# Kernel optimization log

Measured on AMD Instinct MI355X. Metric: run time of the kernel, lower is better.

Reference implementation:

```python
import jax, jax.numpy as jnp
import numpy as np
from functools import partial

L, B, E, H, NL = 512, 16, 768, 12, 12
D = E // H  # head dim = 64
FF = 4 * E
LN_EPS = 1e-5


def gelu_new(x):
    # HF openai-gpt ACT_FNS['gelu'] (tanh approximation)
    c = np.sqrt(2.0 / np.pi).astype(np.float32)
    return 0.5 * x * (1.0 + jnp.tanh(c * (x + 0.044715 * x * x * x)))


def layer_norm(x, g, b):
    mu = jnp.mean(x, axis=-1, keepdims=True)
    var = jnp.mean(jnp.square(x - mu), axis=-1, keepdims=True)
    return (x - mu) * jax.lax.rsqrt(var + LN_EPS) * g + b


def setup_inputs() -> dict:
    key = jax.random.key(0)
    ks = jax.random.split(key, 8)
    s = 0.02
    x = jax.random.normal(ks[0], (L, B, E), dtype=jnp.float32)
    custom_mask = jnp.ones((B, L), dtype=jnp.float32)
    pos_emb = s * jax.random.normal(ks[1], (L, E), dtype=jnp.float32)
    # stacked per-layer params (leading axis = layer)
    params = {
        'c_attn_w': s * jax.random.normal(ks[2], (NL, E, 3 * E), dtype=jnp.float32),
        'c_attn_b': jnp.zeros((NL, 3 * E), dtype=jnp.float32),
        'attn_proj_w': s * jax.random.normal(ks[3], (NL, E, E), dtype=jnp.float32),
        'attn_proj_b': jnp.zeros((NL, E), dtype=jnp.float32),
        'ln1_g': jnp.ones((NL, E), dtype=jnp.float32),
        'ln1_b': jnp.zeros((NL, E), dtype=jnp.float32),
        'c_fc_w': s * jax.random.normal(ks[4], (NL, E, FF), dtype=jnp.float32),
        'c_fc_b': jnp.zeros((NL, FF), dtype=jnp.float32),
        'mlp_proj_w': s * jax.random.normal(ks[5], (NL, FF, E), dtype=jnp.float32),
        'mlp_proj_b': jnp.zeros((NL, E), dtype=jnp.float32),
        'ln2_g': jnp.ones((NL, E), dtype=jnp.float32),
        'ln2_b': jnp.zeros((NL, E), dtype=jnp.float32),
    }
    return {'x': x, 'custom_mask': custom_mask, 'pos_emb': pos_emb, **params}


def _gpt_forward(x, custom_mask, pos_emb, c_attn_w, c_attn_b, attn_proj_w,
                 attn_proj_b, ln1_g, ln1_b, c_fc_w, c_fc_b, mlp_proj_w,
                 mlp_proj_b, ln2_g, ln2_b):
    Lx, Bx, Ex = x.shape
    h = x.transpose(1, 0, 2) + pos_emb[None, :Lx]  # (B, L, E); dropout = eval identity
    # additive padding mask: (1 - m) * finfo.min, broadcast over heads/queries
    add_mask = (1.0 - custom_mask)[:, None, None, :] * jnp.finfo(jnp.float32).min
    causal = jnp.tril(jnp.ones((Lx, Lx), dtype=jnp.float32))  # bias buffer b

    def block(h, p):
        (caw, cab, apw, apb, g1, b1, fw, fb, pw, pb, g2, b2) = p
        qkv = h @ caw + cab                              # (B, L, 3E)
        q, k, v = jnp.split(qkv, 3, axis=-1)
        q = q.reshape(Bx, Lx, H, D).transpose(0, 2, 1, 3)  # (B, H, L, D)
        k = k.reshape(Bx, Lx, H, D).transpose(0, 2, 1, 3)
        v = v.reshape(Bx, Lx, H, D).transpose(0, 2, 1, 3)
        w = jnp.einsum('bhqd,bhkd->bhqk', q, k) / np.float32(np.sqrt(D))
        w = w * causal + (-10000.0) * (1.0 - causal)     # causal bias masking
        w = w + add_mask
        a = jax.nn.softmax(w, axis=-1)
        o = jnp.einsum('bhqk,bhkd->bhqd', a, v)          # (B, H, L, D)
        o = o.transpose(0, 2, 1, 3).reshape(Bx, Lx, Ex)
        a_out = o @ apw + apb
        n = layer_norm(h + a_out, g1, b1)
        m = gelu_new(n @ fw + fb) @ pw + pb
        h2 = layer_norm(n + m, g2, b2)
        return h2, None

    params = (c_attn_w, c_attn_b, attn_proj_w, attn_proj_b, ln1_g, ln1_b,
              c_fc_w, c_fc_b, mlp_proj_w, mlp_proj_b, ln2_g, ln2_b)
    h, _ = jax.lax.scan(block, h, params)
    return h.transpose(1, 0, 2)  # back to (L, B, E)


def reference(x, custom_mask, pos_emb, c_attn_w, c_attn_b, attn_proj_w,
              attn_proj_b, ln1_g, ln1_b, c_fc_w, c_fc_b, mlp_proj_w,
              mlp_proj_b, ln2_g, ln2_b):
    return _gpt_forward(x, custom_mask, pos_emb, c_attn_w, c_attn_b,
                        attn_proj_w, attn_proj_b, ln1_g, ln1_b, c_fc_w,
                        c_fc_b, mlp_proj_w, mlp_proj_b, ln2_g, ln2_b)
```

## Files before the change

### kernel.cpp

```cpp
#include <hip/hip_runtime.h>
#include <cstdint>
#include <cstddef>


#define LSEQ 512
#define NBATCH 16
#define EDIM 768
#define NHEAD 12
#define NLAYER 12

typedef __attribute__((ext_vector_type(8))) short short8;
typedef __attribute__((ext_vector_type(4))) float f32x4;

__device__ __forceinline__ short f2bf(float f) {
  union { float f; unsigned u; } x; x.f = f;
  return (short)((x.u + 0x7FFFu + ((x.u >> 16) & 1u)) >> 16);
}

__device__ __forceinline__ void gload_lds16(const void* g, void* l) {
  __builtin_amdgcn_global_load_lds(
      (__attribute__((address_space(1))) void*)(void*)g,
      (__attribute__((address_space(3))) void*)l, 16, 0, 0);
}

__global__ __launch_bounds__(256) void wt_transpose(const float* __restrict__ W,
                                                    short* __restrict__ Wt,
                                                    int K, int N) {
  __shared__ float tile[32][33];
  const int n0 = blockIdx.x * 32, k0 = blockIdx.y * 32;
  const size_t lo = (size_t)blockIdx.z * K * N;
  const float* Ws = W + lo;
  short* Wd = Wt + lo;
  const int tx = threadIdx.x & 31, ty = threadIdx.x >> 5;
#pragma unroll
  for (int i = 0; i < 4; ++i)
    tile[ty + i * 8][tx] = Ws[(size_t)(k0 + ty + i * 8) * N + n0 + tx];
  __syncthreads();
#pragma unroll
  for (int i = 0; i < 4; ++i)
    Wd[(size_t)(n0 + ty + i * 8) * K + k0 + tx] = f2bf(tile[tx][ty + i * 8]);
}

__global__ __launch_bounds__(256) void embed_k(const float* __restrict__ x,
                                               const float* __restrict__ pos,
                                               float* __restrict__ h,
                                               short* __restrict__ hbf) {
  const int row = blockIdx.x;
  const int b = row >> 9, lp = row & 511;
  const int t = threadIdx.x;
#pragma unroll
  for (int i = 0; i < 3; ++i) {
    const int e = t + i * 256;
    float v = x[(size_t)(lp * 16 + b) * 768 + e] + pos[(size_t)lp * 768 + e];
    h[(size_t)row * 768 + e] = v;
    hbf[(size_t)row * 768 + e] = f2bf(v);
  }
}

__global__ __launch_bounds__(256) void final_k(const float* __restrict__ h,
                                               float* __restrict__ out) {
  const int row = blockIdx.x;
  const int lp = row >> 4, b = row & 15;
  const int t = threadIdx.x;
#pragma unroll
  for (int i = 0; i < 3; ++i) {
    const int e = t + i * 256;
    out[(size_t)row * 768 + e] = h[(size_t)(b * 512 + lp) * 768 + e];
  }
}

__global__ __launch_bounds__(256) void ln_fused(const float* __restrict__ A,
                                                const float* __restrict__ B,
                                                const float* __restrict__ g,
                                                const float* __restrict__ be,
                                                float* __restrict__ outf,
                                                short* __restrict__ outb) {
  const int row = blockIdx.x;
  const int t = threadIdx.x;
  const size_t base = (size_t)row * 768;
  float v[3];
  float s1 = 0.f, s2 = 0.f;
#pragma unroll
  for (int i = 0; i < 3; ++i) {
    const int e = t + i * 256;
    float xv = A[base + e] + B[base + e];
    v[i] = xv; s1 += xv; s2 += xv * xv;
  }
#pragma unroll
  for (int m = 1; m < 64; m <<= 1) {
    s1 += __shfl_xor(s1, m);
    s2 += __shfl_xor(s2, m);
  }
  __shared__ float r1[4], r2[4];
  const int w = t >> 6, l = t & 63;
  if (l == 0) { r1[w] = s1; r2[w] = s2; }
  __syncthreads();
  s1 = r1[0] + r1[1] + r1[2] + r1[3];
  s2 = r2[0] + r2[1] + r2[2] + r2[3];
  const float mu = s1 * (1.f / 768.f);
  const float var = s2 * (1.f / 768.f) - mu * mu;
  const float rs = rsqrtf(var + 1e-5f);
#pragma unroll
  for (int i = 0; i < 3; ++i) {
    const int e = t + i * 256;
    float o = (v[i] - mu) * rs * g[e] + be[e];
    outf[base + e] = o;
    outb[base + e] = f2bf(o);
  }
}

template <int TN, int EPI>
__global__ __launch_bounds__(256) void gemm_bt(const short* __restrict__ A,
                                               const short* __restrict__ Bt,
                                               const float* __restrict__ bias,
                                               void* __restrict__ C,
                                               int N, int K) {
  constexpr int BK = 64;
  __shared__ alignas(16) short Alds[2][128 * BK];
  __shared__ alignas(16) short Blds[2][TN * BK];
  const int t = threadIdx.x;
  const int w = t >> 6, l = t & 63;
  constexpr int WR = (TN == 128) ? 2 : 4;
  constexpr int WC = (TN == 128) ? 2 : 1;
  constexpr int WM = 128 / WR;
  constexpr int MI = WM / 16;
  constexpr int NI = (TN / WC) / 16;
  const int wr = (WC == 2) ? (w >> 1) : w;
  const int wc = (WC == 2) ? (w & 1) : 0;
  const int l15 = l & 15, lhi = l >> 4;
  const int rowA0 = blockIdx.x * 128;
  const int rowB0 = blockIdx.y * TN;
  f32x4 acc[MI][NI];
#pragma unroll
  for (int mi = 0; mi < MI; ++mi)
#pragma unroll
    for (int ni = 0; ni < NI; ++ni) acc[mi][ni] = (f32x4){0.f, 0.f, 0.f, 0.f};

  const int srl = l >> 3;
  const int ss = l & 7;

  const short* aptr[4];
#pragma unroll
  for (int i = 0; i < 4; ++i) {
    const int r = i * 32 + w * 8 + srl;
    aptr[i] = A + (size_t)(rowA0 + r) * K + ((ss ^ (r & 7)) << 3);
  }
  const short* bptr[TN / 32];
#pragma unroll
  for (int i = 0; i < TN / 32; ++i) {
    const int r = i * 32 + w * 8 + srl;
    bptr[i] = Bt + (size_t)(rowB0 + r) * K + ((ss ^ (r & 7)) << 3);
  }

  auto stage = [&](int buf) {
#pragma unroll
    for (int i = 0; i < 4; ++i)
      gload_lds16(aptr[i], &Alds[buf][i * 2048 + w * 512]);
#pragma unroll
    for (int i = 0; i < TN / 32; ++i)
      gload_lds16(bptr[i], &Blds[buf][i * 2048 + w * 512]);
#pragma unroll
    for (int i = 0; i < 4; ++i) aptr[i] += BK;
#pragma unroll
    for (int i = 0; i < TN / 32; ++i) bptr[i] += BK;
  };

  stage(0);
  __syncthreads();

  const int nk = K / BK;
  for (int tt = 0; tt < nk; ++tt) {
    const int cur = tt & 1;
    if (tt + 1 < nk) stage(cur ^ 1);

    short8 af[MI][2], bfr[NI][2];
#pragma unroll
    for (int mi = 0; mi < MI; ++mi) {
      const int r = wr * WM + mi * 16 + l15;
#pragma unroll
      for (int kc = 0; kc < 2; ++kc)
        af[mi][kc] = *(const short8*)
            &Alds[cur][r * 64 + ((((kc << 2) | lhi) ^ (r & 7)) << 3)];
    }
#pragma unroll
    for (int ni = 0; ni < NI; ++ni) {
      const int r = wc * 64 + ni * 16 + l15;
#pragma unroll
      for (int kc = 0; kc < 2; ++kc)
        bfr[ni][kc] = *(const short8*)
            &Blds[cur][r * 64 + ((((kc << 2) | lhi) ^ (r & 7)) << 3)];
    }
#pragma unroll
    for (int mi = 0; mi < MI; ++mi)
#pragma unroll
      for (int ni = 0; ni < NI; ++ni)
#pragma unroll
        for (int kc = 0; kc < 2; ++kc)
          acc[mi][ni] = __builtin_amdgcn_mfma_f32_16x16x32_bf16(
              af[mi][kc], bfr[ni][kc], acc[mi][ni], 0, 0, 0);
    __syncthreads();
  }

  float bv[NI];
#pragma unroll
  for (int ni = 0; ni < NI; ++ni) bv[ni] = bias[rowB0 + wc * 64 + ni * 16 + l15];
#pragma unroll
  for (int mi = 0; mi < MI; ++mi) {
#pragma unroll
    for (int ni = 0; ni < NI; ++ni) {
      const int col = rowB0 + wc * 64 + ni * 16 + l15;
#pragma unroll
      for (int i = 0; i < 4; ++i) {
        const int row = rowA0 + wr * WM + mi * 16 + lhi * 4 + i;
        float v = acc[mi][ni][i] + bv[ni];
        if constexpr (EPI == 0) {
          ((float*)C)[(size_t)row * N + col] = v;
        } else if constexpr (EPI == 1) {
          ((short*)C)[(size_t)row * N + col] = f2bf(v);
        } else {
          float p = v * fmaf(0.044715f, v * v, 1.0f);
          float e = __expf(-1.5957691216057308f * p);
          float r = __builtin_amdgcn_rcpf(1.0f + e);
          ((short*)C)[(size_t)row * N + col] = f2bf(v * r);
        }
      }
    }
  }
}

__global__ __launch_bounds__(256) void attn_k(const short* __restrict__ qkv,
                                              const float* __restrict__ mask,
                                              short* __restrict__ o) {
  const int qb = blockIdx.x;
  const int hh = blockIdx.y;
  const int b = blockIdx.z;
  const int t = threadIdx.x, w = t >> 6, l = t & 63;
  const int l15 = l & 15, lhi = l >> 4;
  __shared__ alignas(16) short Klds[64 * 64];
  __shared__ alignas(16) short Vlds[64 * 64];
  __shared__ alignas(16) short Plds[4][16 * 72];

  short8 qa[2];
  {
    const size_t base =
        (size_t)(b * LSEQ + qb * 64 + w * 16 + l15) * 2304 + hh * 64;
    qa[0] = *(const short8*)&qkv[base + lhi * 8];
    qa[1] = *(const short8*)&qkv[base + 32 + lhi * 8];
  }
  float mrow[4] = {-1e30f, -1e30f, -1e30f, -1e30f};
  float lrow[4] = {0.f, 0.f, 0.f, 0.f};
  const f32x4 zero4 = {0.f, 0.f, 0.f, 0.f};
  f32x4 oacc[4];
#pragma unroll
  for (int nt = 0; nt < 4; ++nt) oacc[nt] = zero4;

  const int nkt = qb + 1;
  for (int kt = 0; kt < nkt; ++kt) {
    __syncthreads();
    {
      const int kr = t >> 2, cc = (t & 3) * 16;
      const size_t grow = (size_t)(b * LSEQ + kt * 64 + kr) * 2304 + hh * 64;
      short8 k0 = *(const short8*)&qkv[grow + 768 + cc];
      short8 k1 = *(const short8*)&qkv[grow + 768 + cc + 8];
      short8 v0 = *(const short8*)&qkv[grow + 1536 + cc];
      short8 v1 = *(const short8*)&qkv[grow + 1536 + cc + 8];
      const int sw = (kr & 7) << 4;
      *(short8*)((char*)Klds + ((kr * 128 + cc * 2) ^ sw)) = k0;
      *(short8*)((char*)Klds + ((kr * 128 + cc * 2 + 16) ^ sw)) = k1;
#pragma unroll
      for (int e = 0; e < 8; ++e) {
        const int n0 = cc + e, n1 = cc + 8 + e;
        ((short*)Vlds)[((n0 * 128 + kr * 2) ^ ((n0 & 7) << 4)) >> 1] = v0[e];
        ((short*)Vlds)[((n1 * 128 + kr * 2) ^ ((n1 & 7) << 4)) >> 1] = v1[e];
      }
    }
    __syncthreads();

    f32x4 s[4];
#pragma unroll
    for (int jt = 0; jt < 4; ++jt) {
      f32x4 z = zero4;
#pragma unroll
      for (int kc = 0; kc < 2; ++kc) {
        const int rowk = jt * 16 + l15;
        short8 kb = *(const short8*)((char*)Klds +
                     ((rowk * 128 + kc * 64 + lhi * 16) ^ ((rowk & 7) << 4)));
        z = __builtin_amdgcn_mfma_f32_16x16x32_bf16(qa[kc], kb, z, 0, 0, 0);
      }
      s[jt] = z;
    }

    float addm[4];
#pragma unroll
    for (int jt = 0; jt < 4; ++jt)
      addm[jt] = (1.0f - mask[b * LSEQ + kt * 64 + jt * 16 + l15]) *
                 -3.402823466e38f;
#pragma unroll
    for (int jt = 0; jt < 4; ++jt) {
      const int colg = kt * 64 + jt * 16 + l15;
#pragma unroll
      for (int i = 0; i < 4; ++i) {
        const int rowg = qb * 64 + w * 16 + lhi * 4 + i;
        float sv = s[jt][i] * 0.125f;
        if (colg > rowg) sv = -10000.0f;
        s[jt][i] = sv + addm[jt];
      }
    }

    float mnew[4], sc[4];
#pragma unroll
    for (int i = 0; i < 4; ++i) {
      float tm = fmaxf(fmaxf(s[0][i], s[1][i]), fmaxf(s[2][i], s[3][i]));
#pragma unroll
      for (int mm = 1; mm < 16; mm <<= 1) tm = fmaxf(tm, __shfl_xor(tm, mm));
      mnew[i] = fmaxf(mrow[i], tm);
      sc[i] = __expf(mrow[i] - mnew[i]);
      mrow[i] = mnew[i];
    }
#pragma unroll
    for (int i = 0; i < 4; ++i) {
      float ts = 0.f;
#pragma unroll
      for (int jt = 0; jt < 4; ++jt) {
        float p = __expf(s[jt][i] - mnew[i]);
        s[jt][i] = p;
        ts += p;
      }
#pragma unroll
      for (int mm = 1; mm < 16; mm <<= 1) ts += __shfl_xor(ts, mm);
      lrow[i] = lrow[i] * sc[i] + ts;
      oacc[0][i] *= sc[i]; oacc[1][i] *= sc[i];
      oacc[2][i] *= sc[i]; oacc[3][i] *= sc[i];
    }

    short* Pw = &Plds[w][0];
#pragma unroll
    for (int jt = 0; jt < 4; ++jt)
#pragma unroll
      for (int i = 0; i < 4; ++i)
        Pw[(lhi * 4 + i) * 72 + jt * 16 + l15] = f2bf(s[jt][i]);
    __syncthreads();
    short8 pa[2];
#pragma unroll
    for (int kc = 0; kc < 2; ++kc)
      pa[kc] = *(const short8*)&Pw[l15 * 72 + kc * 32 + lhi * 8];

#pragma unroll
    for (int nt = 0; nt < 4; ++nt) {
#pragma unroll
      for (int kc = 0; kc < 2; ++kc) {
        const int rown = nt * 16 + l15;
        short8 vb = *(const short8*)((char*)Vlds +
                     ((rown * 128 + kc * 64 + lhi * 16) ^ ((rown & 7) << 4)));
        oacc[nt] = __builtin_amdgcn_mfma_f32_16x16x32_bf16(pa[kc], vb,
                                                           oacc[nt], 0, 0, 0);
      }
    }
  }

#pragma unroll
  for (int i = 0; i < 4; ++i) {
    const size_t row = (size_t)(b * LSEQ + qb * 64 + w * 16 + lhi * 4 + i);
    const float inv = 1.0f / lrow[i];
#pragma unroll
    for (int nt = 0; nt < 4; ++nt)
      o[row * 768 + hh * 64 + nt * 16 + l15] = f2bf(oacc[nt][i] * inv);
  }
}

extern "C" void kernel_launch(void* const* d_in, const int* in_sizes, int n_in,
                              void* d_out, int out_size, void* d_ws,
                              size_t ws_size, hipStream_t stream) {
  const float* x    = (const float*)d_in[0];
  const float* mask = (const float*)d_in[1];
  const float* pos  = (const float*)d_in[2];
  const float* caw  = (const float*)d_in[3];
  const float* cab  = (const float*)d_in[4];
  const float* apw  = (const float*)d_in[5];
  const float* apb  = (const float*)d_in[6];
  const float* g1   = (const float*)d_in[7];
  const float* b1   = (const float*)d_in[8];
  const float* fw   = (const float*)d_in[9];
  const float* fb   = (const float*)d_in[10];
  const float* pw   = (const float*)d_in[11];
  const float* pb   = (const float*)d_in[12];
  const float* g2   = (const float*)d_in[13];
  const float* b2   = (const float*)d_in[14];

  char* ws = (char*)d_ws;
  size_t off = 0;
  auto alloc = [&](size_t bytes) {
    size_t o = off;
    off += (bytes + 255) & ~(size_t)255;
    return o;
  };
  float* h    = (float*)(ws + alloc(8192ull * 768 * 4));
  short* hbf  = (short*)(ws + alloc(8192ull * 768 * 2));
  float* nrm  = (float*)(ws + alloc(8192ull * 768 * 4));
  short* nbf  = (short*)(ws + alloc(8192ull * 768 * 2));
  short* qkvb = (short*)(ws + alloc(8192ull * 2304 * 2));
  short* obf  = (short*)(ws + alloc(8192ull * 768 * 2));
  float* aout = (float*)(ws + alloc(8192ull * 768 * 4));
  short* gbf  = (short*)(ws + alloc(8192ull * 3072 * 2));
  short* wt_attn = (short*)(ws + alloc(12ull * 768 * 2304 * 2));
  short* wt_proj = (short*)(ws + alloc(12ull * 768 * 768 * 2));
  short* wt_fc   = (short*)(ws + alloc(12ull * 768 * 3072 * 2));
  short* wt_mlp  = (short*)(ws + alloc(12ull * 3072 * 768 * 2));
  (void)ws_size; (void)in_sizes; (void)n_in; (void)out_size;

  wt_transpose<<<dim3(2304 / 32, 768 / 32, 12), 256, 0, stream>>>(caw, wt_attn, 768, 2304);
  wt_transpose<<<dim3(768 / 32, 768 / 32, 12), 256, 0, stream>>>(apw, wt_proj, 768, 768);
  wt_transpose<<<dim3(3072 / 32, 768 / 32, 12), 256, 0, stream>>>(fw, wt_fc, 768, 3072);
  wt_transpose<<<dim3(768 / 32, 3072 / 32, 12), 256, 0, stream>>>(pw, wt_mlp, 3072, 768);

  embed_k<<<8192, 256, 0, stream>>>(x, pos, h, hbf);

  for (int L = 0; L < 12; ++L) {
    gemm_bt<128, 1><<<dim3(64, 18), 256, 0, stream>>>(
        hbf, wt_attn + (size_t)L * 2304 * 768, cab + (size_t)L * 2304, qkvb, 2304, 768);
    attn_k<<<dim3(8, 12, 16), 256, 0, stream>>>(qkvb, mask, obf);
    gemm_bt<64, 0><<<dim3(64, 12), 256, 0, stream>>>(
        obf, wt_proj + (size_t)L * 768 * 768, apb + (size_t)L * 768, aout, 768, 768);
    ln_fused<<<8192, 256, 0, stream>>>(h, aout, g1 + (size_t)L * 768,
                                       b1 + (size_t)L * 768, nrm, nbf);
    gemm_bt<128, 2><<<dim3(64, 24), 256, 0, stream>>>(
        nbf, wt_fc + (size_t)L * 768 * 3072, fb + (size_t)L * 3072, gbf, 3072, 768);
    gemm_bt<64, 0><<<dim3(64, 12), 256, 0, stream>>>(
        gbf, wt_mlp + (size_t)L * 3072 * 768, pb + (size_t)L * 768, aout, 768, 3072);
    ln_fused<<<8192, 256, 0, stream>>>(nrm, aout, g2 + (size_t)L * 768,
                                       b2 + (size_t)L * 768, h, hbf);
  }

  final_k<<<8192, 256, 0, stream>>>(h, (float*)d_out);
}
```

Measured before the change: 3.485 ms.

## Use triple-buffered BK=32 GEMM pipeline with explicit vmcnt waits and raised MFMA priority

Reworks the bf16 GEMM main loop from a double-buffered BK=64 scheme into a three-stage ring of BK=32 LDS buffers. Explicit s_waitcnt vmcnt and s_barrier calls let up to two tiles of global-to-LDS loads stay in flight while MFMAs run, and the LDS swizzle is adapted to 32-wide rows. s_setprio is raised around the MFMA block. The aim is to hide global memory latency better, at the cost of twice as many iterations, an extra barrier per iteration, and fragile hand-written wait counts.

```diff
diff --git a/kernel.cpp b/kernel.cpp
--- a/kernel.cpp
+++ b/kernel.cpp
@@ -21,6 +21,11 @@
   __builtin_amdgcn_global_load_lds(
       (__attribute__((address_space(1))) void*)(void*)g,
       (__attribute__((address_space(3))) void*)l, 16, 0, 0);
+}
+
+template <int N>
+__device__ __forceinline__ void waitvm() {
+  asm volatile("s_waitcnt vmcnt(%0)" ::"n"(N) : "memory");
 }
 
 __global__ __launch_bounds__(256) void wt_transpose(const float* __restrict__ W,
@@ -115,9 +120,13 @@
                                                const float* __restrict__ bias,
                                                void* __restrict__ C,
                                                int N, int K) {
-  constexpr int BK = 64;
-  __shared__ alignas(16) short Alds[2][128 * BK];
-  __shared__ alignas(16) short Blds[2][TN * BK];
+  constexpr int BK = 32;
+  constexpr int NB = 3;
+  constexpr int LA = 2;
+  constexpr int LB = TN / 64;
+  constexpr int L = LA + LB;
+  __shared__ alignas(16) short Alds[NB][128 * BK];
+  __shared__ alignas(16) short Blds[NB][TN * BK];
   const int t = threadIdx.x;
   const int w = t >> 6, l = t & 63;
   constexpr int WR = (TN == 128) ? 2 : 4;
@@ -136,69 +145,74 @@
 #pragma unroll
     for (int ni = 0; ni < NI; ++ni) acc[mi][ni] = (f32x4){0.f, 0.f, 0.f, 0.f};
 
-  const int srl = l >> 3;
-  const int ss = l & 7;
-
-  const short* aptr[4];
-#pragma unroll
-  for (int i = 0; i < 4; ++i) {
-    const int r = i * 32 + w * 8 + srl;
-    aptr[i] = A + (size_t)(rowA0 + r) * K + ((ss ^ (r & 7)) << 3);
-  }
-  const short* bptr[TN / 32];
-#pragma unroll
-  for (int i = 0; i < TN / 32; ++i) {
-    const int r = i * 32 + w * 8 + srl;
-    bptr[i] = Bt + (size_t)(rowB0 + r) * K + ((ss ^ (r & 7)) << 3);
+  const int srl = w * 16 + (l >> 2);
+  const int sa = l & 3;
+
+  const short* aptr[LA];
+#pragma unroll
+  for (int i = 0; i < LA; ++i) {
+    const int r = i * 64 + srl;
+    aptr[i] = A + (size_t)(rowA0 + r) * K + ((sa ^ ((r >> 1) & 3)) << 3);
+  }
+  const short* bptr[LB];
+#pragma unroll
+  for (int i = 0; i < LB; ++i) {
+    const int r = i * 64 + srl;
+    bptr[i] = Bt + (size_t)(rowB0 + r) * K + ((sa ^ ((r >> 1) & 3)) << 3);
   }
 
   auto stage = [&](int buf) {
 #pragma unroll
-    for (int i = 0; i < 4; ++i)
-      gload_lds16(aptr[i], &Alds[buf][i * 2048 + w * 512]);
-#pragma unroll
-    for (int i = 0; i < TN / 32; ++i)
-      gload_lds16(bptr[i], &Blds[buf][i * 2048 + w * 512]);
-#pragma unroll
-    for (int i = 0; i < 4; ++i) aptr[i] += BK;
-#pragma unroll
-    for (int i = 0; i < TN / 32; ++i) bptr[i] += BK;
+    for (int i = 0; i < LA; ++i)
+      gload_lds16(aptr[i], &Alds[buf][(i * 64 + w * 16) * BK]);
+#pragma unroll
+    for (int i = 0; i < LB; ++i)
+      gload_lds16(bptr[i], &Blds[buf][(i * 64 + w * 16) * BK]);
+#pragma unroll
+    for (int i = 0; i < LA; ++i) aptr[i] += BK;
+#pragma unroll
+    for (int i = 0; i < LB; ++i) bptr[i] += BK;
   };
 
+  const int nk = K / BK;
   stage(0);
-  __syncthreads();
-
-  const int nk = K / BK;
+  stage(1);
+  stage(2);
+
+  int c = 0;
   for (int tt = 0; tt < nk; ++tt) {
-    const int cur = tt & 1;
-    if (tt + 1 < nk) stage(cur ^ 1);
-
-    short8 af[MI][2], bfr[NI][2];
+    if (tt < nk - 2) waitvm<2 * L>();
+    else if (tt == nk - 2) waitvm<L>();
+    else waitvm<0>();
+    asm volatile("s_barrier" ::: "memory");
+
+    short8 af[MI], bfr[NI];
 #pragma unroll
     for (int mi = 0; mi < MI; ++mi) {
       const int r = wr * WM + mi * 16 + l15;
-#pragma unroll
-      for (int kc = 0; kc < 2; ++kc)
-        af[mi][kc] = *(const short8*)
-            &Alds[cur][r * 64 + ((((kc << 2) | lhi) ^ (r & 7)) << 3)];
+      af[mi] = *(const short8*)&Alds[c][r * BK + ((lhi ^ ((r >> 1) & 3)) << 3)];
     }
 #pragma unroll
     for (int ni = 0; ni < NI; ++ni) {
       const int r = wc * 64 + ni * 16 + l15;
-#pragma unroll
-      for (int kc = 0; kc < 2; ++kc)
-        bfr[ni][kc] = *(const short8*)
-            &Blds[cur][r * 64 + ((((kc << 2) | lhi) ^ (r & 7)) << 3)];
-    }
+      bfr[ni] = *(const short8*)&Blds[c][r * BK + ((lhi ^ ((r >> 1) & 3)) << 3)];
+    }
+    asm volatile("s_waitcnt lgkmcnt(0)" ::: "memory");
+    __builtin_amdgcn_sched_barrier(0);
+    asm volatile("s_barrier" ::: "memory");
+
+    if (tt + 3 < nk) stage(c);
+
+    __builtin_amdgcn_s_setprio(1);
 #pragma unroll
     for (int mi = 0; mi < MI; ++mi)
 #pragma unroll
       for (int ni = 0; ni < NI; ++ni)
-#pragma unroll
-        for (int kc = 0; kc < 2; ++kc)
-          acc[mi][ni] = __builtin_amdgcn_mfma_f32_16x16x32_bf16(
-              af[mi][kc], bfr[ni][kc], acc[mi][ni], 0, 0, 0);
-    __syncthreads();
+        acc[mi][ni] = __builtin_amdgcn_mfma_f32_16x16x32_bf16(
+            af[mi], bfr[ni], acc[mi][ni], 0, 0, 0);
+    __builtin_amdgcn_s_setprio(0);
+
+    c = (c == NB - 1) ? 0 : c + 1;
   }
 
   float bv[NI];
```

Result: no change. 3.455 ms (-0.9%).
